# Kernel tuning notes

Hardware: AMD Instinct MI355X
Metric: run time of the kernel (lower is better)

Reference implementation:

```python
import jax, jax.numpy as jnp
import numpy as np

THRESH = 0.3
OUT_THRESH = 0.3
LENS = 0.5  # surrogate-gradient window (ActFun in snn-delays repo)


@jax.custom_vjp
def spike(x):
    # Heaviside spike with rectangular surrogate gradient
    return (x > 0.0).astype(x.dtype)

def _spike_fwd(x):
    return spike(x), x

def _spike_bwd(x, g):
    return (g * (jnp.abs(x) < LENS).astype(g.dtype),)

spike.defvjp(_spike_fwd, _spike_bwd)


def setup_inputs() -> dict:
    key = jax.random.key(0)
    ks = jax.random.split(key, 7)
    B, T, I, H, O = 256, 50, 1024, 2048, 20
    # binary input spikes (rate ~0.2), as an SNN would receive
    inp = (jax.random.uniform(ks[0], (B, T, I)) < 0.2).astype(jnp.float32)
    # Linear(in, out, bias=False) -> weight [out, in], Kaiming-uniform-ish init
    w_ih = jax.random.uniform(ks[1], (H, I), minval=-1.0, maxval=1.0) / np.sqrt(I)
    w_hh = jax.random.uniform(ks[2], (H, H), minval=-1.0, maxval=1.0) / np.sqrt(H)
    w_ho = jax.random.uniform(ks[3], (O, H), minval=-1.0, maxval=1.0) / np.sqrt(H)
    tau_m_h = 0.83 + 0.1 * jax.random.normal(ks[4], (H,))
    tau_m_o = 0.83 + 0.1 * jax.random.normal(ks[5], (O,))
    return {"input": inp, "w_ih": w_ih, "w_hh": w_hh, "w_ho": w_ho,
            "tau_m_h": tau_m_h, "tau_m_o": tau_m_o}


def _rsnn_forward(inp, w_ih, w_hh, w_ho, tau_m_h, tau_m_o):
    B, T, I = inp.shape
    H = w_ih.shape[0]
    O = w_ho.shape[0]
    alpha_h = jnp.exp(-1.0 / tau_m_h)  # [H]
    alpha_o = jnp.exp(-1.0 / tau_m_o)  # [O]
    zH = jnp.zeros((B, H), inp.dtype)
    zO = jnp.zeros((B, O), inp.dtype)

    def step(carry, x_t):
        h_mem, h_spk, o_mem, o_spk, o_sum, mot = carry
        # hidden membrane update: input + recurrent + decayed (reset-gated) mem
        h_mem = (x_t @ w_ih.T) + (h_spk @ w_hh.T) + h_mem * alpha_h * (1.0 - h_spk)
        h_spk = spike(h_mem - THRESH)
        # output membrane update
        o_mem = o_mem * alpha_o * (1.0 - o_spk) + h_spk @ w_ho.T
        o_spk = spike(o_mem - OUT_THRESH)
        o_sum = o_sum + o_spk
        mot = mot + jax.nn.softmax(o_mem, axis=1)
        return (h_mem, h_spk, o_mem, o_spk, o_sum, mot), None

    init = (zH, zH, zO, zO, zO, zO)
    (h_mem, h_spk, o_mem, o_spk, o_sum, mot), _ = jax.lax.scan(
        step, init, jnp.swapaxes(inp, 0, 1))  # scan over time [T,B,I]
    return o_sum / T, mot


def reference(input, w_ih, w_hh, w_ho, tau_m_h, tau_m_o):
    return _rsnn_forward(input, w_ih, w_hh, w_ho, tau_m_h, tau_m_o)
```

## Files before the change

kernel.cpp:

```cpp
#include <hip/hip_runtime.h>
#include <stdint.h>
#include <math.h>


#define B_   256
#define T_   50
#define I_   1024
#define H_   2048
#define O_   20
#define XIN_T  262144
#define XS_BUF 524288
#define WNT 294912
#define WPL 98304

typedef __attribute__((ext_vector_type(4))) int intx4;
typedef long long ll_t;

__device__ __forceinline__ int digit_of(float v, int p) {
  int W = (int)rintf(v * 134217728.0f);
  int c0 = ((W + 128) & 255) - 128;
  int W1 = (W - c0) >> 8;
  int c1 = ((W1 + 128) & 255) - 128;
  int W2 = (W1 - c1) >> 8;
  return (p == 0) ? c0 : (p == 1) ? c1 : W2;
}

__global__ void prep_w(const float* __restrict__ w_ih,
                       const float* __restrict__ w_hh,
                       int8_t* __restrict__ Wtl) {
  int blk = blockIdx.x;
  int n = blk / 9, kg = blk % 9;
  int k9 = (kg * 256 + (int)threadIdx.x) * 4;
  int p = k9 / 3072, kk = k9 % 3072;
  const float* src = (kk < 1024) ? (w_ih + n * I_ + kk)
                                 : (w_hh + n * H_ + (kk - 1024));
  float4 v = *(const float4*)src;
  int d0 = digit_of(v.x, p) & 255;
  int d1 = digit_of(v.y, p) & 255;
  int d2 = digit_of(v.z, p) & 255;
  int d3 = digit_of(v.w, p) & 255;
  int packed = d0 | (d1 << 8) | (d2 << 16) | (d3 << 24);
  size_t off = (size_t)(n >> 5) * WNT + (size_t)p * WPL + (kk >> 6) * 2048 +
               (n & 31) * 64 + (kk & 63);
  *(int*)(Wtl + off) = packed;
}

__global__ void init_k(int8_t* __restrict__ Xin, int8_t* __restrict__ Xs,
                       float* __restrict__ Hm, const float* __restrict__ input,
                       const float* __restrict__ tau_h,
                       const float* __restrict__ tau_o,
                       float* __restrict__ AlphaH, float* __restrict__ AlphaO,
                       const float* __restrict__ w_ho, double* __restrict__ WhoD,
                       float* __restrict__ Om, float* __restrict__ Osp,
                       float* __restrict__ Osu, float* __restrict__ Mo) {
  int id = blockIdx.x * 256 + threadIdx.x;
  {
    int b = id >> 8, i4 = (id & 255) * 4;
    for (int t = 0; t < T_; ++t) {
      float4 v = *(const float4*)(input + ((size_t)(b * T_ + t) << 10) + i4);
      uchar4 pk;
      pk.x = v.x > 0.5f ? 1 : 0;
      pk.y = v.y > 0.5f ? 1 : 0;
      pk.z = v.z > 0.5f ? 1 : 0;
      pk.w = v.w > 0.5f ? 1 : 0;
      *(uchar4*)(Xin + (size_t)t * XIN_T + (b >> 6) * 65536 + (i4 >> 6) * 4096 +
                 (b & 63) * 64 + (i4 & 63)) = pk;
    }
  }
  *(double*)(Xs + (size_t)id * 8) = 0.0;
  *(float4*)(Hm + (size_t)id * 8) = make_float4(0.f, 0.f, 0.f, 0.f);
  *(float4*)(Hm + (size_t)id * 8 + 4) = make_float4(0.f, 0.f, 0.f, 0.f);
  if (id < 64 * O_ * 32) {
    int nt = id / 640, rem = id % 640, o = rem / 32, hl = rem & 31;
    WhoD[id] = (double)w_ho[o * H_ + nt * 32 + hl];
  }
  if (id < H_) AlphaH[id] = (float)exp((double)(-1.0f / tau_h[id]));
  if (id < O_) AlphaO[id] = (float)exp((double)(-1.0f / tau_o[id]));
  if (id < B_ * O_) {
    Om[id] = 0.f; Osp[id] = 0.f; Osu[id] = 0.f; Mo[id] = 0.f;
  }
}

__global__ __launch_bounds__(512, 4) void step_k(
    const int8_t* __restrict__ Wtl, const int8_t* __restrict__ Xin,
    int8_t* __restrict__ Xs, float* __restrict__ Hm, double* __restrict__ Po,
    const double* __restrict__ WhoD, const float* __restrict__ AlphaH,
    const float* __restrict__ AlphaO, float* __restrict__ Om,
    float* __restrict__ Osp, float* __restrict__ Osu, float* __restrict__ Mo,
    int t) {
  __shared__ double WhoL[640];
  __shared__ __align__(16) int8_t red[49152];
  __shared__ int8_t spk_lT[1024];
  __shared__ float om_l[O_];

  const int j = blockIdx.x;
  const int nt = (j & 7) * 8 + ((j >> 3) & 7);
  const int mt = j >> 6;
  const int tid = threadIdx.x;
  const int l = tid & 63, k = tid >> 6;
  const int r_ = l & 15, q = l >> 4;

  for (int i = tid; i < 640; i += 512) WhoL[i] = WhoD[nt * 640 + i];

  if (t > 0 && j < B_ && tid < O_) {
    const double* pp = Po + ((size_t)(((t - 1) & 1) * 256 + j) * 64) * 20 + tid;
    double s = 0.0;
#pragma unroll
    for (int n2 = 0; n2 < 64; ++n2) s += pp[n2 * 20];
    float r = (float)s;
    float m = Om[j * O_ + tid] * AlphaO[tid] * (1.0f - Osp[j * O_ + tid]) + r;
    om_l[tid] = m;
  }
  __syncthreads();
  if (t > 0 && j < B_ && tid < O_) {
    float m = om_l[tid];
    float mx = om_l[0];
#pragma unroll
    for (int o = 1; o < O_; ++o) mx = fmaxf(mx, om_l[o]);
    float se = 0.f;
#pragma unroll
    for (int o = 0; o < O_; ++o) se += expf(om_l[o] - mx);
    float sp = (m - 0.3f) > 0.f ? 1.f : 0.f;
    Om[j * O_ + tid] = m;
    Osp[j * O_ + tid] = sp;
    Osu[j * O_ + tid] += sp;
    Mo[j * O_ + tid] += expf(m - mx) / se;
  }

  const int arow = ((mt & 1) * 32 + r_) * 64 + q * 16;
  const int8_t* Ain = Xin + (size_t)t * XIN_T + (mt >> 1) * 65536 + arow;
  const int8_t* Asp = Xs + (size_t)(t & 1) * XS_BUF + (mt >> 1) * 131072 + arow;
  const int8_t* Bw = Wtl + (size_t)nt * WNT + r_ * 64 + q * 16;
  const int u0 = k * 6;

  intx4 acc[2][2][3];
#pragma unroll
  for (int fr = 0; fr < 2; ++fr)
#pragma unroll
    for (int fc = 0; fc < 2; ++fc)
#pragma unroll
      for (int p = 0; p < 3; ++p) acc[fr][fc][p] = (intx4){0, 0, 0, 0};

  intx4 a[2][2], b[2][2][3];
  {
    const int8_t* ap = (u0 < 16) ? (Ain + u0 * 4096) : (Asp + (u0 - 16) * 4096);
    a[0][0] = *(const intx4*)ap;
    a[0][1] = *(const intx4*)(ap + 1024);
    const int8_t* bp = Bw + u0 * 2048;
#pragma unroll
    for (int p = 0; p < 3; ++p)
#pragma unroll
      for (int fc = 0; fc < 2; ++fc)
        b[0][fc][p] = *(const intx4*)(bp + p * WPL + fc * 1024);
  }
#pragma unroll
  for (int i = 0; i < 6; ++i) {
    const int cur = i & 1, nxt = cur ^ 1;
    if (i < 5) {
      const int un = u0 + i + 1;
      const int8_t* ap = (un < 16) ? (Ain + un * 4096) : (Asp + (un - 16) * 4096);
      a[nxt][0] = *(const intx4*)ap;
      a[nxt][1] = *(const intx4*)(ap + 1024);
      const int8_t* bp = Bw + un * 2048;
#pragma unroll
      for (int p = 0; p < 3; ++p)
#pragma unroll
        for (int fc = 0; fc < 2; ++fc)
          b[nxt][fc][p] = *(const intx4*)(bp + p * WPL + fc * 1024);
    }
#pragma unroll
    for (int p = 0; p < 3; ++p)
#pragma unroll
      for (int fc = 0; fc < 2; ++fc) {
        acc[0][fc][p] = __builtin_amdgcn_mfma_i32_16x16x64_i8(
            a[cur][0], b[cur][fc][p], acc[0][fc][p], 0, 0, 0);
        acc[1][fc][p] = __builtin_amdgcn_mfma_i32_16x16x64_i8(
            a[cur][1], b[cur][fc][p], acc[1][fc][p], 0, 0, 0);
      }
  }

#define REDP(slot, idx) (red + (((slot) * 12 + (idx)) * 64 + l) * 16)
#define ACCIDX(fr, fc, p) ((fr) * 6 + (fc) * 3 + (p))
  if (k & 1) {
#pragma unroll
    for (int fr = 0; fr < 2; ++fr)
#pragma unroll
      for (int fc = 0; fc < 2; ++fc)
#pragma unroll
        for (int p = 0; p < 3; ++p)
          *(intx4*)REDP(k >> 1, ACCIDX(fr, fc, p)) = acc[fr][fc][p];
  }
  __syncthreads();
  if (!(k & 1)) {
#pragma unroll
    for (int fr = 0; fr < 2; ++fr)
#pragma unroll
      for (int fc = 0; fc < 2; ++fc)
#pragma unroll
        for (int p = 0; p < 3; ++p)
          acc[fr][fc][p] =
              acc[fr][fc][p] + *(const intx4*)REDP(k >> 1, ACCIDX(fr, fc, p));
  }
  __syncthreads();
  if (k == 2 || k == 6) {
#pragma unroll
    for (int fr = 0; fr < 2; ++fr)
#pragma unroll
      for (int fc = 0; fc < 2; ++fc)
#pragma unroll
        for (int p = 0; p < 3; ++p)
          *(intx4*)REDP(k >> 2, ACCIDX(fr, fc, p)) = acc[fr][fc][p];
  }
  __syncthreads();
  if (k == 0 || k == 4) {
#pragma unroll
    for (int fr = 0; fr < 2; ++fr)
#pragma unroll
      for (int fc = 0; fc < 2; ++fc)
#pragma unroll
        for (int p = 0; p < 3; ++p)
          acc[fr][fc][p] =
              acc[fr][fc][p] + *(const intx4*)REDP(k >> 2, ACCIDX(fr, fc, p));
  }
  __syncthreads();
  if (k == 4) {
#pragma unroll
    for (int fr = 0; fr < 2; ++fr)
#pragma unroll
      for (int fc = 0; fc < 2; ++fc)
#pragma unroll
        for (int p = 0; p < 3; ++p)
          *(intx4*)REDP(0, ACCIDX(fr, fc, p)) = acc[fr][fc][p];
  }
  __syncthreads();

  if (k == 0) {
    int8_t* Xw = Xs + (size_t)((t + 1) & 1) * XS_BUF;
#pragma unroll
    for (int fc = 0; fc < 2; ++fc) {
      const int h = nt * 32 + fc * 16 + r_;
      const float alpha = AlphaH[h];
#pragma unroll
      for (int fr = 0; fr < 2; ++fr) {
        intx4 s0 = acc[fr][fc][0] + *(const intx4*)REDP(0, ACCIDX(fr, fc, 0));
        intx4 s1 = acc[fr][fc][1] + *(const intx4*)REDP(0, ACCIDX(fr, fc, 1));
        intx4 s2 = acc[fr][fc][2] + *(const intx4*)REDP(0, ACCIDX(fr, fc, 2));
        unsigned spkpack = 0;
#pragma unroll
        for (int jj = 0; jj < 4; ++jj) {
          ll_t Sv = (ll_t)s0[jj] + ((ll_t)s1[jj] << 8) + ((ll_t)s2[jj] << 16);
          float M = (float)((double)Sv * 7.450580596923828125e-9);
          const int brow = mt * 32 + fr * 16 + q * 4 + jj;
          const int idx = brow * H_ + h;
          float hp = Hm[idx];
          float spf = (hp - 0.3f) > 0.f ? 1.f : 0.f;
          float hm = M + hp * alpha * (1.0f - spf);
          Hm[idx] = hm;
          unsigned spk = (hm - 0.3f) > 0.f ? 1u : 0u;
          Xw[(brow >> 6) * 131072 + (h >> 6) * 4096 + (brow & 63) * 64 +
             (h & 63)] = (int8_t)spk;
          spkpack |= spk << (8 * jj);
        }
        *(unsigned*)(spk_lT + (fc * 16 + r_) * 32 + fr * 16 + q * 4) = spkpack;
      }
    }
  }
  __syncthreads();

  if (tid < 128) {
    const int bl = tid >> 2, og = (tid & 3) * 5;
    const double* W0 = WhoL + og * 32;
    double a0 = 0, a1 = 0, a2 = 0, a3 = 0, a4 = 0;
#pragma unroll
    for (int hl = 0; hl < 32; ++hl) {
      double m = (double)spk_lT[hl * 32 + bl];
      a0 += m * W0[hl];
      a1 += m * W0[32 + hl];
      a2 += m * W0[64 + hl];
      a3 += m * W0[96 + hl];
      a4 += m * W0[128 + hl];
    }
    double* dst =
        Po + ((size_t)((t & 1) * 256 + mt * 32 + bl) * 64 + nt) * 20 + og;
    dst[0] = a0; dst[1] = a1; dst[2] = a2; dst[3] = a3; dst[4] = a4;
  }
#undef REDP
#undef ACCIDX
}

__global__ void final_k(const double* __restrict__ Po,
                        const float* __restrict__ AlphaO,
                        const float* __restrict__ Om,
                        const float* __restrict__ Osp,
                        const float* __restrict__ Osu,
                        const float* __restrict__ Mo, float* __restrict__ out) {
  __shared__ float om_l[O_];
  const int j = blockIdx.x, tid = threadIdx.x;
  if (tid < O_) {
    const double* pp = Po + ((size_t)(256 + j) * 64) * 20 + tid;
    double s = 0.0;
#pragma unroll
    for (int n2 = 0; n2 < 64; ++n2) s += pp[n2 * 20];
    float r = (float)s;
    float m = Om[j * O_ + tid] * AlphaO[tid] * (1.0f - Osp[j * O_ + tid]) + r;
    om_l[tid] = m;
  }
  __syncthreads();
  if (tid < O_) {
    float m = om_l[tid];
    float mx = om_l[0];
#pragma unroll
    for (int o = 1; o < O_; ++o) mx = fmaxf(mx, om_l[o]);
    float se = 0.f;
#pragma unroll
    for (int o = 0; o < O_; ++o) se += expf(om_l[o] - mx);
    float sp = (m - 0.3f) > 0.f ? 1.f : 0.f;
    out[j * O_ + tid] = (Osu[j * O_ + tid] + sp) / 50.0f;
    out[B_ * O_ + j * O_ + tid] = Mo[j * O_ + tid] + expf(m - mx) / se;
  }
}

extern "C" void kernel_launch(void* const* d_in, const int* in_sizes, int n_in,
                              void* d_out, int out_size, void* d_ws, size_t ws_size,
                              hipStream_t stream) {
  const float* input = (const float*)d_in[0];
  const float* w_ih  = (const float*)d_in[1];
  const float* w_hh  = (const float*)d_in[2];
  const float* w_ho  = (const float*)d_in[3];
  const float* tau_h = (const float*)d_in[4];
  const float* tau_o = (const float*)d_in[5];

  char* ws = (char*)d_ws;
  int8_t* Wtl    = (int8_t*)(ws);
  int8_t* Xin    = (int8_t*)(ws + 18874368);
  int8_t* Xs     = (int8_t*)(ws + 31981568);
  double* Po     = (double*)(ws + 33030144);
  float*  Hm     = (float*)(ws + 38273024);
  double* WhoD   = (double*)(ws + 40370176);
  float*  AlphaH = (float*)(ws + 40697856);
  float*  AlphaO = (float*)(ws + 40706048);
  float*  Om     = (float*)(ws + 40706176);
  float*  Osp    = (float*)(ws + 40726656);
  float*  Osu    = (float*)(ws + 40747136);
  float*  Mo     = (float*)(ws + 40767616);
  float*  out    = (float*)d_out;

  prep_w<<<2048 * 9, 256, 0, stream>>>(w_ih, w_hh, Wtl);
  init_k<<<256, 256, 0, stream>>>(Xin, Xs, Hm, input, tau_h, tau_o, AlphaH,
                                  AlphaO, w_ho, WhoD, Om, Osp, Osu, Mo);
  for (int t = 0; t < T_; ++t) {
    step_k<<<512, 512, 0, stream>>>(Wtl, Xin, Xs, Hm, Po, WhoD, AlphaH, AlphaO,
                                    Om, Osp, Osu, Mo, t);
  }
  final_k<<<256, 64, 0, stream>>>(Po, AlphaO, Om, Osp, Osu, Mo, out);
}
```

Baseline: 1.107 ms.

## Double per-block batch tile to 64 rows and flatten split-K reduction

```diff
diff --git a/kernel.cpp b/kernel.cpp
--- a/kernel.cpp
+++ b/kernel.cpp
@@ -81,7 +81,7 @@
   }
 }
 
-__global__ __launch_bounds__(512, 4) void step_k(
+__global__ __launch_bounds__(512, 2) void step_k(
     const int8_t* __restrict__ Wtl, const int8_t* __restrict__ Xin,
     int8_t* __restrict__ Xs, float* __restrict__ Hm, double* __restrict__ Po,
     const double* __restrict__ WhoD, const float* __restrict__ AlphaH,
@@ -89,63 +89,36 @@
     float* __restrict__ Osp, float* __restrict__ Osu, float* __restrict__ Mo,
     int t) {
   __shared__ double WhoL[640];
-  __shared__ __align__(16) int8_t red[49152];
-  __shared__ int8_t spk_lT[1024];
-  __shared__ float om_l[O_];
+  __shared__ __align__(16) int8_t red[98304];
+  __shared__ int8_t spk_lT[2048];
 
   const int j = blockIdx.x;
   const int nt = (j & 7) * 8 + ((j >> 3) & 7);
-  const int mt = j >> 6;
+  const int mg = j >> 6;
   const int tid = threadIdx.x;
   const int l = tid & 63, k = tid >> 6;
   const int r_ = l & 15, q = l >> 4;
 
   for (int i = tid; i < 640; i += 512) WhoL[i] = WhoD[nt * 640 + i];
 
-  if (t > 0 && j < B_ && tid < O_) {
-    const double* pp = Po + ((size_t)(((t - 1) & 1) * 256 + j) * 64) * 20 + tid;
-    double s = 0.0;
-#pragma unroll
-    for (int n2 = 0; n2 < 64; ++n2) s += pp[n2 * 20];
-    float r = (float)s;
-    float m = Om[j * O_ + tid] * AlphaO[tid] * (1.0f - Osp[j * O_ + tid]) + r;
-    om_l[tid] = m;
-  }
-  __syncthreads();
-  if (t > 0 && j < B_ && tid < O_) {
-    float m = om_l[tid];
-    float mx = om_l[0];
-#pragma unroll
-    for (int o = 1; o < O_; ++o) mx = fmaxf(mx, om_l[o]);
-    float se = 0.f;
-#pragma unroll
-    for (int o = 0; o < O_; ++o) se += expf(om_l[o] - mx);
-    float sp = (m - 0.3f) > 0.f ? 1.f : 0.f;
-    Om[j * O_ + tid] = m;
-    Osp[j * O_ + tid] = sp;
-    Osu[j * O_ + tid] += sp;
-    Mo[j * O_ + tid] += expf(m - mx) / se;
-  }
-
-  const int arow = ((mt & 1) * 32 + r_) * 64 + q * 16;
-  const int8_t* Ain = Xin + (size_t)t * XIN_T + (mt >> 1) * 65536 + arow;
-  const int8_t* Asp = Xs + (size_t)(t & 1) * XS_BUF + (mt >> 1) * 131072 + arow;
+  const int8_t* Ain = Xin + (size_t)t * XIN_T + mg * 65536 + r_ * 64 + q * 16;
+  const int8_t* Asp = Xs + (size_t)(t & 1) * XS_BUF + mg * 131072 + r_ * 64 + q * 16;
   const int8_t* Bw = Wtl + (size_t)nt * WNT + r_ * 64 + q * 16;
   const int u0 = k * 6;
 
-  intx4 acc[2][2][3];
-#pragma unroll
-  for (int fr = 0; fr < 2; ++fr)
+  intx4 acc[4][2][3];
+#pragma unroll
+  for (int fr = 0; fr < 4; ++fr)
 #pragma unroll
     for (int fc = 0; fc < 2; ++fc)
 #pragma unroll
       for (int p = 0; p < 3; ++p) acc[fr][fc][p] = (intx4){0, 0, 0, 0};
 
-  intx4 a[2][2], b[2][2][3];
+  intx4 a[2][4], b[2][2][3];
   {
     const int8_t* ap = (u0 < 16) ? (Ain + u0 * 4096) : (Asp + (u0 - 16) * 4096);
-    a[0][0] = *(const intx4*)ap;
-    a[0][1] = *(const intx4*)(ap + 1024);
+#pragma unroll
+    for (int fr = 0; fr < 4; ++fr) a[0][fr] = *(const intx4*)(ap + fr * 1024);
     const int8_t* bp = Bw + u0 * 2048;
 #pragma unroll
     for (int p = 0; p < 3; ++p)
@@ -159,8 +132,8 @@
     if (i < 5) {
       const int un = u0 + i + 1;
       const int8_t* ap = (un < 16) ? (Ain + un * 4096) : (Asp + (un - 16) * 4096);
-      a[nxt][0] = *(const intx4*)ap;
-      a[nxt][1] = *(const intx4*)(ap + 1024);
+#pragma unroll
+      for (int fr = 0; fr < 4; ++fr) a[nxt][fr] = *(const intx4*)(ap + fr * 1024);
       const int8_t* bp = Bw + un * 2048;
 #pragma unroll
       for (int p = 0; p < 3; ++p)
@@ -169,111 +142,89 @@
           b[nxt][fc][p] = *(const intx4*)(bp + p * WPL + fc * 1024);
     }
 #pragma unroll
-    for (int p = 0; p < 3; ++p)
-#pragma unroll
-      for (int fc = 0; fc < 2; ++fc) {
-        acc[0][fc][p] = __builtin_amdgcn_mfma_i32_16x16x64_i8(
-            a[cur][0], b[cur][fc][p], acc[0][fc][p], 0, 0, 0);
-        acc[1][fc][p] = __builtin_amdgcn_mfma_i32_16x16x64_i8(
-            a[cur][1], b[cur][fc][p], acc[1][fc][p], 0, 0, 0);
-      }
-  }
-
-#define REDP(slot, idx) (red + (((slot) * 12 + (idx)) * 64 + l) * 16)
-#define ACCIDX(fr, fc, p) ((fr) * 6 + (fc) * 3 + (p))
-  if (k & 1) {
-#pragma unroll
-    for (int fr = 0; fr < 2; ++fr)
+    for (int fr = 0; fr < 4; ++fr)
 #pragma unroll
       for (int fc = 0; fc < 2; ++fc)
 #pragma unroll
         for (int p = 0; p < 3; ++p)
-          *(intx4*)REDP(k >> 1, ACCIDX(fr, fc, p)) = acc[fr][fc][p];
-  }
-  __syncthreads();
-  if (!(k & 1)) {
-#pragma unroll
-    for (int fr = 0; fr < 2; ++fr)
-#pragma unroll
-      for (int fc = 0; fc < 2; ++fc)
-#pragma unroll
-        for (int p = 0; p < 3; ++p)
-          acc[fr][fc][p] =
-              acc[fr][fc][p] + *(const intx4*)REDP(k >> 1, ACCIDX(fr, fc, p));
-  }
-  __syncthreads();
-  if (k == 2 || k == 6) {
-#pragma unroll
-    for (int fr = 0; fr < 2; ++fr)
-#pragma unroll
-      for (int fc = 0; fc < 2; ++fc)
-#pragma unroll
-        for (int p = 0; p < 3; ++p)
-          *(intx4*)REDP(k >> 2, ACCIDX(fr, fc, p)) = acc[fr][fc][p];
-  }
-  __syncthreads();
-  if (k == 0 || k == 4) {
-#pragma unroll
-    for (int fr = 0; fr < 2; ++fr)
-#pragma unroll
-      for (int fc = 0; fc < 2; ++fc)
-#pragma unroll
-        for (int p = 0; p < 3; ++p)
-          acc[fr][fc][p] =
-              acc[fr][fc][p] + *(const intx4*)REDP(k >> 2, ACCIDX(fr, fc, p));
-  }
-  __syncthreads();
-  if (k == 4) {
-#pragma unroll
-    for (int fr = 0; fr < 2; ++fr)
-#pragma unroll
-      for (int fc = 0; fc < 2; ++fc)
-#pragma unroll
-        for (int p = 0; p < 3; ++p)
-          *(intx4*)REDP(0, ACCIDX(fr, fc, p)) = acc[fr][fc][p];
-  }
-  __syncthreads();
-
-  if (k == 0) {
-    int8_t* Xw = Xs + (size_t)((t + 1) & 1) * XS_BUF;
-#pragma unroll
-    for (int fc = 0; fc < 2; ++fc) {
-      const int h = nt * 32 + fc * 16 + r_;
-      const float alpha = AlphaH[h];
-#pragma unroll
-      for (int fr = 0; fr < 2; ++fr) {
-        intx4 s0 = acc[fr][fc][0] + *(const intx4*)REDP(0, ACCIDX(fr, fc, 0));
-        intx4 s1 = acc[fr][fc][1] + *(const intx4*)REDP(0, ACCIDX(fr, fc, 1));
-        intx4 s2 = acc[fr][fc][2] + *(const intx4*)REDP(0, ACCIDX(fr, fc, 2));
-        unsigned spkpack = 0;
-#pragma unroll
-        for (int jj = 0; jj < 4; ++jj) {
-          ll_t Sv = (ll_t)s0[jj] + ((ll_t)s1[jj] << 8) + ((ll_t)s2[jj] << 16);
-          float M = (float)((double)Sv * 7.450580596923828125e-9);
-          const int brow = mt * 32 + fr * 16 + q * 4 + jj;
-          const int idx = brow * H_ + h;
-          float hp = Hm[idx];
-          float spf = (hp - 0.3f) > 0.f ? 1.f : 0.f;
-          float hm = M + hp * alpha * (1.0f - spf);
-          Hm[idx] = hm;
-          unsigned spk = (hm - 0.3f) > 0.f ? 1u : 0u;
-          Xw[(brow >> 6) * 131072 + (h >> 6) * 4096 + (brow & 63) * 64 +
-             (h & 63)] = (int8_t)spk;
-          spkpack |= spk << (8 * jj);
-        }
-        *(unsigned*)(spk_lT + (fc * 16 + r_) * 32 + fr * 16 + q * 4) = spkpack;
-      }
-    }
-  }
-  __syncthreads();
-
-  if (tid < 128) {
+          acc[fr][fc][p] = __builtin_amdgcn_mfma_i32_16x16x64_i8(
+              a[cur][fr], b[cur][fc][p], acc[fr][fc][p], 0, 0, 0);
+  }
+
+#define REDP(w, idx) (red + (((w) * 12 + (idx)) * 64 + l) * 16)
+
+  int8_t* Xw = Xs + (size_t)((t + 1) & 1) * XS_BUF;
+  auto epilogue = [&](intx4 s0, intx4 s1, intx4 s2, int fr_e, int fc_e) {
+    const int h = nt * 32 + fc_e * 16 + r_;
+    const float alpha = AlphaH[h];
+    unsigned spkpack = 0;
+#pragma unroll
+    for (int jj = 0; jj < 4; ++jj) {
+      ll_t Sv = (ll_t)s0[jj] + ((ll_t)s1[jj] << 8) + ((ll_t)s2[jj] << 16);
+      float M = (float)((double)Sv * 7.450580596923828125e-9);
+      const int brl = fr_e * 16 + q * 4 + jj;
+      const int idx = (mg * 64 + brl) * H_ + h;
+      float hp = Hm[idx];
+      float spf = (hp - 0.3f) > 0.f ? 1.f : 0.f;
+      float hm = M + hp * alpha * (1.0f - spf);
+      Hm[idx] = hm;
+      unsigned spk = (hm - 0.3f) > 0.f ? 1u : 0u;
+      Xw[mg * 131072 + (h >> 6) * 4096 + brl * 64 + (h & 63)] = (int8_t)spk;
+      spkpack |= spk << (8 * jj);
+    }
+    *(unsigned*)(spk_lT + (fc_e * 16 + r_) * 64 + fr_e * 16 + q * 4) = spkpack;
+  };
+
+#pragma unroll
+  for (int fr = 0; fr < 2; ++fr)
+#pragma unroll
+    for (int fc = 0; fc < 2; ++fc)
+#pragma unroll
+      for (int p = 0; p < 3; ++p)
+        *(intx4*)REDP(k, (fr * 2 + fc) * 3 + p) = acc[fr][fc][p];
+  __syncthreads();
+  if (k < 4) {
+    const int fr_e = k >> 1, fc_e = k & 1;
+    const int base = (fr_e * 2 + fc_e) * 3;
+    intx4 s0 = (intx4){0, 0, 0, 0}, s1 = s0, s2 = s0;
+#pragma unroll
+    for (int w = 0; w < 8; ++w) {
+      s0 = s0 + *(const intx4*)REDP(w, base + 0);
+      s1 = s1 + *(const intx4*)REDP(w, base + 1);
+      s2 = s2 + *(const intx4*)REDP(w, base + 2);
+    }
+    epilogue(s0, s1, s2, fr_e, fc_e);
+  }
+  __syncthreads();
+#pragma unroll
+  for (int fr = 0; fr < 2; ++fr)
+#pragma unroll
+    for (int fc = 0; fc < 2; ++fc)
+#pragma unroll
+      for (int p = 0; p < 3; ++p)
+        *(intx4*)REDP(k, (fr * 2 + fc) * 3 + p) = acc[2 + fr][fc][p];
+  __syncthreads();
+  if (k >= 4) {
+    const int fr_e = 2 + ((k - 4) >> 1), fc_e = k & 1;
+    const int base = ((fr_e - 2) * 2 + fc_e) * 3;
+    intx4 s0 = (intx4){0, 0, 0, 0}, s1 = s0, s2 = s0;
+#pragma unroll
+    for (int w = 0; w < 8; ++w) {
+      s0 = s0 + *(const intx4*)REDP(w, base + 0);
+      s1 = s1 + *(const intx4*)REDP(w, base + 1);
+      s2 = s2 + *(const intx4*)REDP(w, base + 2);
+    }
+    epilogue(s0, s1, s2, fr_e, fc_e);
+  }
+  __syncthreads();
+
+  if (tid < 256) {
     const int bl = tid >> 2, og = (tid & 3) * 5;
     const double* W0 = WhoL + og * 32;
     double a0 = 0, a1 = 0, a2 = 0, a3 = 0, a4 = 0;
 #pragma unroll
     for (int hl = 0; hl < 32; ++hl) {
-      double m = (double)spk_lT[hl * 32 + bl];
+      double m = (double)spk_lT[hl * 64 + bl];
       a0 += m * W0[hl];
       a1 += m * W0[32 + hl];
       a2 += m * W0[64 + hl];
@@ -281,11 +232,34 @@
       a4 += m * W0[128 + hl];
     }
     double* dst =
-        Po + ((size_t)((t & 1) * 256 + mt * 32 + bl) * 64 + nt) * 20 + og;
+        Po + ((size_t)((t & 1) * 256 + mg * 64 + bl) * 64 + nt) * 20 + og;
     dst[0] = a0; dst[1] = a1; dst[2] = a2; dst[3] = a3; dst[4] = a4;
+  } else if (k == 7 && t > 0) {
+    float m = -3.0e38f;
+    if (l < 20) {
+      const double* pp = Po + ((size_t)(((t - 1) & 1) * 256 + j) * 64) * 20 + l;
+      double s = 0.0;
+#pragma unroll
+      for (int n2 = 0; n2 < 64; ++n2) s += pp[n2 * 20];
+      m = Om[j * O_ + l] * AlphaO[l] * (1.0f - Osp[j * O_ + l]) + (float)s;
+    }
+    float mx = m;
+#pragma unroll
+    for (int off = 16; off > 0; off >>= 1)
+      mx = fmaxf(mx, __shfl_xor(mx, off, 32));
+    float eo = (l < 20) ? expf(m - mx) : 0.f;
+    float se = eo;
+#pragma unroll
+    for (int off = 16; off > 0; off >>= 1) se += __shfl_xor(se, off, 32);
+    if (l < 20) {
+      float sp = (m - 0.3f) > 0.f ? 1.f : 0.f;
+      Om[j * O_ + l] = m;
+      Osp[j * O_ + l] = sp;
+      Osu[j * O_ + l] += sp;
+      Mo[j * O_ + l] += eo / se;
+    }
   }
 #undef REDP
-#undef ACCIDX
 }
 
 __global__ void final_k(const double* __restrict__ Po,
@@ -349,7 +323,7 @@
   init_k<<<256, 256, 0, stream>>>(Xin, Xs, Hm, input, tau_h, tau_o, AlphaH,
                                   AlphaO, w_ho, WhoD, Om, Osp, Osu, Mo);
   for (int t = 0; t < T_; ++t) {
-    step_k<<<512, 512, 0, stream>>>(Wtl, Xin, Xs, Hm, Po, WhoD, AlphaH, AlphaO,
+    step_k<<<256, 512, 0, stream>>>(Wtl, Xin, Xs, Hm, Po, WhoD, AlphaH, AlphaO,
                                     Om, Osp, Osu, Mo, t);
   }
   final_k<<<256, 64, 0, stream>>>(Po, AlphaO, Om, Osp, Osu, Mo, out);
```

After: 900.8 us. -18.7%, faster.
